# Kernel optimization log

Hardware: AMD Instinct MI355X
Metric: run time of the kernel (lower is better)

The kernel has to match this reference:

```python
import jax, jax.numpy as jnp
import numpy as np

B, T, D, H, KH, HD, F, L, V = 2, 2048, 1024, 16, 4, 64, 4096, 4, 32000
G = H // KH  # num_key_value_groups
EPS = 1e-6
SCALE = HD ** -0.5


def setup_inputs() -> dict:
    key = jax.random.key(0)
    ks = jax.random.split(key, 8)
    std = 0.02
    return {
        "input_ids": jax.random.randint(ks[0], (B, T), 0, V, dtype=jnp.int32),
        "embed_w": jax.random.normal(ks[1], (V, D), jnp.float32) * std,
        "pos_w": jax.random.normal(ks[2], (T, D), jnp.float32) * std,
        "ln1_w": jnp.ones((L, D), jnp.float32),
        "ln2_w": jnp.ones((L, D), jnp.float32),
        "wq": jax.random.normal(ks[3], (L, D, H * HD), jnp.float32) * std,
        "wkv": jax.random.normal(ks[4], (L, D, 2 * KH * HD), jnp.float32) * std,
        "wo": jax.random.normal(ks[5], (L, H * HD, D), jnp.float32) * std,
        "w1": jax.random.normal(ks[6], (L, D, F), jnp.float32) * std,
        "w2": jax.random.normal(ks[7], (L, F, D), jnp.float32) * std,
        "norm_w": jnp.ones((D,), jnp.float32),
    }


def _rmsnorm(x, w):
    return x * jax.lax.rsqrt(jnp.mean(x * x, axis=-1, keepdims=True) + EPS) * w


def reference(input_ids, embed_w, pos_w, ln1_w, ln2_w, wq, wkv, wo, w1, w2, norm_w):
    causal = jnp.tril(jnp.ones((T, T), dtype=bool))  # True = keep
    x = embed_w[input_ids] + pos_w[:T]  # [B,T,D]
    for l in range(L):
        h = _rmsnorm(x, ln1_w[l])
        q = (h @ wq[l]).reshape(B, T, H, HD)
        kv = h @ wkv[l]
        k, v = jnp.split(kv, 2, axis=-1)
        k = jnp.repeat(k.reshape(B, T, KH, HD), G, axis=2)  # GQA repeat_interleave
        v = jnp.repeat(v.reshape(B, T, KH, HD), G, axis=2)
        scores = jnp.einsum("bqhd,bkhd->bhqk", q, k) * SCALE
        scores = jnp.where(causal, scores, -jnp.inf)
        p = jax.nn.softmax(scores, axis=-1)
        o = jnp.einsum("bhqk,bkhd->bqhd", p, v).reshape(B, T, H * HD)
        x = x + o @ wo[l]
        h = _rmsnorm(x, ln2_w[l])
        x = x + jax.nn.gelu(h @ w1[l], approximate=False) @ w2[l]
    x = _rmsnorm(x, norm_w)
    logits = x @ embed_w.T  # tied lm_head
    return logits
```

## Files before the change

kernel.cpp:

```cpp
#include <hip/hip_runtime.h>
#include <hip/hip_bf16.h>

#define DI __device__ __forceinline__

typedef unsigned short u16;
typedef unsigned int u32;
typedef __attribute__((ext_vector_type(8))) short bf16x8;
typedef __attribute__((ext_vector_type(4))) float f32x4;

#define B_   2
#define T_   2048
#define D_   1024
#define H_   16
#define KH_  4
#define HD_  64
#define F_   4096
#define L_   4
#define V_   32000
#define M_   (B_ * T_)
#define QKVN (H_*HD_ + 2*KH_*HD_)

DI u16 f2bf(float f) {
  __hip_bfloat16 h = __float2bfloat16(f);
  return *reinterpret_cast<u16*>(&h);
}

DI float bf2f(u16 b) {
  __hip_bfloat16 h = *reinterpret_cast<__hip_bfloat16*>(&b);
  return __bfloat162float(h);
}

DI void gl_lds16(const void* g, void* l) {
  __builtin_amdgcn_global_load_lds(
      (const __attribute__((address_space(1))) u32*)g,
      (__attribute__((address_space(3))) u32*)l, 16, 0, 0);
}

#define BARRIER() do { asm volatile("" ::: "memory"); __builtin_amdgcn_s_barrier(); asm volatile("" ::: "memory"); } while (0)
#define LGK0()    asm volatile("s_waitcnt lgkmcnt(0)" ::: "memory")
#define VMC(n)    asm volatile("s_waitcnt vmcnt(" #n ")" ::: "memory")
#define PRIO(p)   __builtin_amdgcn_s_setprio(p)

__global__ __launch_bounds__(256) void embed_kernel(const int* __restrict__ ids,
                                                    const float* __restrict__ ew,
                                                    const float* __restrict__ pw,
                                                    float* __restrict__ x) {
  const int row = blockIdx.x;
  const int t = row & (T_ - 1);
  const int id = ids[row];
  float4 e = reinterpret_cast<const float4*>(ew + (size_t)id * D_)[threadIdx.x];
  float4 p = reinterpret_cast<const float4*>(pw + (size_t)t * D_)[threadIdx.x];
  e.x += p.x; e.y += p.y; e.z += p.z; e.w += p.w;
  reinterpret_cast<float4*>(x + (size_t)row * D_)[threadIdx.x] = e;
}

__global__ __launch_bounds__(256) void conv_kernel(const float* __restrict__ W,
                                                   u16* __restrict__ Wb) {
  const size_t i = (size_t)blockIdx.x * 256 + threadIdx.x;
  float4 v = reinterpret_cast<const float4*>(W)[i];
  ushort4 ov;
  ov.x = f2bf(v.x); ov.y = f2bf(v.y); ov.z = f2bf(v.z); ov.w = f2bf(v.w);
  reinterpret_cast<ushort4*>(Wb)[i] = ov;
}

__global__ __launch_bounds__(256) void convt_fused(const float* __restrict__ wq,
                                                   const float* __restrict__ wkv,
                                                   const float* __restrict__ wo,
                                                   const float* __restrict__ w1,
                                                   const float* __restrict__ w2,
                                                   u16* __restrict__ wtq,
                                                   u16* __restrict__ wto,
                                                   u16* __restrict__ wt1,
                                                   u16* __restrict__ wt2) {
  const int t = blockIdx.x;
  const float* W; u16* Wt; int K, N, local;
  if (t < 1024)      { W = wq;  Wt = wtq;               K = 1024; N = 1024; local = t; }
  else if (t < 1536) { W = wkv; Wt = wtq + 1024*1024;   K = 1024; N = 512;  local = t - 1024; }
  else if (t < 2560) { W = wo;  Wt = wto;               K = 1024; N = 1024; local = t - 1536; }
  else if (t < 6656) { W = w1;  Wt = wt1;               K = 1024; N = 4096; local = t - 2560; }
  else               { W = w2;  Wt = wt2;               K = 4096; N = 1024; local = t - 6656; }
  const int nk = K >> 5;
  const int k0 = (local % nk) * 32, n0 = (local / nk) * 32;
  __shared__ float tb[32][33];
  const int tx = threadIdx.x & 31, ty = threadIdx.x >> 5;
  #pragma unroll
  for (int i = 0; i < 4; i++)
    tb[ty + i*8][tx] = W[(size_t)(k0 + ty + i*8) * N + n0 + tx];
  __syncthreads();
  #pragma unroll
  for (int i = 0; i < 4; i++)
    Wt[(size_t)(n0 + ty + i*8) * K + k0 + tx] = f2bf(tb[tx][ty + i*8]);
}

__global__ __launch_bounds__(256) void rmsnorm_kernel(const float* __restrict__ x,
                                                      const float* __restrict__ w,
                                                      u16* __restrict__ out) {
  const int row = blockIdx.x;
  const int tid = threadIdx.x;
  float4 v = reinterpret_cast<const float4*>(x + (size_t)row * D_)[tid];
  float ss = v.x*v.x + v.y*v.y + v.z*v.z + v.w*v.w;
  #pragma unroll
  for (int off = 32; off > 0; off >>= 1) ss += __shfl_down(ss, off, 64);
  __shared__ float red[4];
  if ((tid & 63) == 0) red[tid >> 6] = ss;
  __syncthreads();
  const float tot = red[0] + red[1] + red[2] + red[3];
  const float rstd = rsqrtf(tot * (1.0f / D_) + 1e-6f);
  float4 wv = reinterpret_cast<const float4*>(w)[tid];
  ushort4 ov;
  ov.x = f2bf(v.x * rstd * wv.x);
  ov.y = f2bf(v.y * rstd * wv.y);
  ov.z = f2bf(v.z * rstd * wv.z);
  ov.w = f2bf(v.w * rstd * wv.w);
  reinterpret_cast<ushort4*>(out + (size_t)row * D_)[tid] = ov;
}

template <int EPI>
__global__ __launch_bounds__(256) void gemm_bt(const u16* __restrict__ A,
                                               const u16* __restrict__ Bt,
                                               const float* __restrict__ res,
                                               u16* __restrict__ Cb,
                                               float* __restrict__ Cf,
                                               int M, int N, int K) {
  __shared__ u16 As[128 * 64];
  __shared__ u16 Bs[128 * 64];
  const int tid = threadIdx.x;
  const int n0 = blockIdx.x * 128;
  const int m0 = blockIdx.y * 128;
  const int lane = tid & 63, wave = tid >> 6;
  const int wm = wave >> 1, wn = wave & 1;
  const int l15 = lane & 15, l4 = lane >> 4;
  const int srow = tid >> 3, scol = (tid & 7) * 8;
  const u16* ag = A + (size_t)(m0 + srow) * K + scol;
  const u16* bg = Bt + (size_t)(n0 + srow) * K + scol;
  u16* asd = &As[srow * 64 + scol];
  u16* bsd = &Bs[srow * 64 + scol];
  f32x4 acc[4][4] = {};
  const int nk = K >> 6;
  for (int kt = 0; kt < nk; kt++) {
    const int k0 = kt * 64;
    __syncthreads();
    #pragma unroll
    for (int i = 0; i < 4; i++) gl_lds16(ag + (size_t)i*32*K + k0, asd + i*32*64);
    #pragma unroll
    for (int i = 0; i < 4; i++) gl_lds16(bg + (size_t)i*32*K + k0, bsd + i*32*64);
    __syncthreads();
    #pragma unroll
    for (int s = 0; s < 2; s++) {
      bf16x8 af[4], bfv[4];
      #pragma unroll
      for (int i = 0; i < 4; i++)
        af[i] = *reinterpret_cast<const bf16x8*>(&As[(wm*64 + i*16 + l15)*64 + s*32 + l4*8]);
      #pragma unroll
      for (int j = 0; j < 4; j++)
        bfv[j] = *reinterpret_cast<const bf16x8*>(&Bs[(wn*64 + j*16 + l15)*64 + s*32 + l4*8]);
      #pragma unroll
      for (int i = 0; i < 4; i++)
        #pragma unroll
        for (int j = 0; j < 4; j++)
          acc[i][j] = __builtin_amdgcn_mfma_f32_16x16x32_bf16(bfv[j], af[i], acc[i][j], 0, 0, 0);
    }
  }
  #pragma unroll
  for (int i = 0; i < 4; i++) {
    const int row = m0 + wm*64 + i*16 + l15;
    #pragma unroll
    for (int j = 0; j < 4; j++) {
      const int colb = n0 + wn*64 + j*16 + l4*4;
      const size_t idx = (size_t)row * N + colb;
      const f32x4 v = acc[i][j];
      if (EPI == 0) {
        ushort4 ov;
        ov.x = f2bf(v[0]); ov.y = f2bf(v[1]); ov.z = f2bf(v[2]); ov.w = f2bf(v[3]);
        *reinterpret_cast<ushort4*>(&Cb[idx]) = ov;
      } else {
        const float4 rv = *reinterpret_cast<const float4*>(&res[idx]);
        float4 ov;
        ov.x = v[0] + rv.x; ov.y = v[1] + rv.y; ov.z = v[2] + rv.z; ov.w = v[3] + rv.w;
        *reinterpret_cast<float4*>(&Cf[idx]) = ov;
      }
    }
  }
}

template <int EPI>
__global__ __launch_bounds__(512, 2) void gemm256(const u16* __restrict__ A,
                                                  const u16* __restrict__ Bt,
                                                  u16* __restrict__ Cb,
                                                  float* __restrict__ Cf,
                                                  int M, int N, int K) {
  __shared__ char lds[131072];
  char* const AsB = lds;
  char* const BsB = lds + 65536;
  const int tid = threadIdx.x;
  const int lane = tid & 63, wave = tid >> 6;
  const int wm = wave >> 2, wn = wave & 3;
  const int l15 = lane & 15, l4 = lane >> 4;

  const int nm = M >> 8;
  const int nwg = nm * (N >> 8);
  const int cpx = nwg >> 3;
  const int bid = blockIdx.x;
  const int wg = (bid & 7) * cpx + (bid >> 3);
  const int m0 = (wg % nm) << 8;
  const int n0 = (wg / nm) << 8;

  const u16* const Atile = A + (size_t)m0 * K;
  const u16* const Btile = Bt + (size_t)n0 * K;

  int soff[2][2], pd[2][2];
  #pragma unroll
  for (int h = 0; h < 2; ++h)
    #pragma unroll
    for (int jj = 0; jj < 2; ++jj) {
      const int row = h*128 + jj*64 + (tid >> 3);
      const int sl  = (tid & 7) ^ (row & 7);
      soff[h][jj] = row * K + sl * 8;
      pd[h][jj]   = h*16384 + jj*8192 + tid*16;
    }
  const int swz = (l15 & 7) << 4;
  const int rb0 = l15*128 + ((l4*16)      ^ swz);
  const int rb1 = l15*128 + ((64 + l4*16) ^ swz);

  #define STA(S,H,T) do { const u16* g_ = Atile + (T)*64; char* d_ = AsB + (S)*32768; \
      gl_lds16(g_ + soff[H][0], d_ + pd[H][0]); gl_lds16(g_ + soff[H][1], d_ + pd[H][1]); } while (0)
  #define STB(S,H,T) do { const u16* g_ = Btile + (T)*64; char* d_ = BsB + (S)*32768; \
      gl_lds16(g_ + soff[H][0], d_ + pd[H][0]); gl_lds16(g_ + soff[H][1], d_ + pd[H][1]); } while (0)
  #define RDA(S,GI,RB) (*reinterpret_cast<const bf16x8*>(AsB + (S)*32768 + (GI)*2048 + (RB)))
  #define RDB(S,GJ,RB) (*reinterpret_cast<const bf16x8*>(BsB + (S)*32768 + (GJ)*2048 + (RB)))

  f32x4 acc[8][4] = {};
  bf16x8 Ar[4][2], Br[4][2];

  #define RDA03(S) { _Pragma("unroll") for (int i=0;i<4;++i){ Ar[i][0]=RDA(S,i*2+wm,rb0); Ar[i][1]=RDA(S,i*2+wm,rb1);} }
  #define RDA47(S) { _Pragma("unroll") for (int i=0;i<4;++i){ Ar[i][0]=RDA(S,(i+4)*2+wm,rb0); Ar[i][1]=RDA(S,(i+4)*2+wm,rb1);} }
  #define RDB01(S) { _Pragma("unroll") for (int j=0;j<2;++j){ Br[j][0]=RDB(S,j*4+wn,rb0); Br[j][1]=RDB(S,j*4+wn,rb1);} }
  #define RDB23(S) { _Pragma("unroll") for (int j=2;j<4;++j){ Br[j][0]=RDB(S,j*4+wn,rb0); Br[j][1]=RDB(S,j*4+wn,rb1);} }
  #define MFQ(IO,JL) { _Pragma("unroll") for (int i=0;i<4;++i) _Pragma("unroll") for (int jj=0;jj<2;++jj) { \
      acc[(IO)+i][(JL)+jj] = __builtin_amdgcn_mfma_f32_16x16x32_bf16(Br[(JL)+jj][0], Ar[i][0], acc[(IO)+i][(JL)+jj],0,0,0); \
      acc[(IO)+i][(JL)+jj] = __builtin_amdgcn_mfma_f32_16x16x32_bf16(Br[(JL)+jj][1], Ar[i][1], acc[(IO)+i][(JL)+jj],0,0,0); } }

  STA(0,0,0); STA(0,1,0); STB(0,0,0); STB(0,1,0);
  VMC(4);
  STA(1,0,1); STB(1,0,1); STB(1,1,1);
  VMC(6);
  BARRIER();

  const int niter = K >> 7;
  for (int it = 0; it < niter; ++it) {
    const int t0 = it*2, t1 = t0 + 1;
    const bool pf = (it + 1 < niter);
    RDA03(0); RDB01(0); STA(1,1,t1);
    BARRIER(); LGK0(); PRIO(1); MFQ(0,0); PRIO(0); BARRIER();
    RDB23(0); if (pf) STA(0,0,t0+2);
    BARRIER(); LGK0(); PRIO(1); MFQ(0,2); PRIO(0); BARRIER();
    RDA47(0); if (pf) STB(0,0,t0+2);
    BARRIER(); LGK0(); PRIO(1); MFQ(4,0); PRIO(0); BARRIER();
    if (pf) { STB(0,1,t0+2); VMC(6); } else { VMC(0); }
    BARRIER(); PRIO(1); MFQ(4,2); PRIO(0); BARRIER();
    RDA03(1); RDB01(1); if (pf) STA(0,1,t0+2);
    BARRIER(); LGK0(); PRIO(1); MFQ(0,0); PRIO(0); BARRIER();
    RDB23(1); if (pf) STA(1,0,t1+2);
    BARRIER(); LGK0(); PRIO(1); MFQ(0,2); PRIO(0); BARRIER();
    RDA47(1); if (pf) STB(1,0,t1+2);
    BARRIER(); LGK0(); PRIO(1); MFQ(4,0); PRIO(0); BARRIER();
    if (pf) { STB(1,1,t1+2); VMC(6); }
    BARRIER(); PRIO(1); MFQ(4,2); PRIO(0); BARRIER();
  }

  #pragma unroll
  for (int i = 0; i < 8; ++i) {
    const int row = m0 + (i*2 + wm)*16 + l15;
    #pragma unroll
    for (int j = 0; j < 4; ++j) {
      const int colb = n0 + (j*4 + wn)*16 + l4*4;
      const f32x4 v = acc[i][j];
      if (EPI == 0) {
        *reinterpret_cast<f32x4*>(&Cf[(size_t)row * N + colb]) = v;
      } else {
        ushort4 ov;
        #pragma unroll
        for (int rr = 0; rr < 4; ++rr) {
          const float g = 0.5f * v[rr] * (1.0f + erff(v[rr] * 0.70710678118f));
          ((u16*)&ov)[rr] = f2bf(g);
        }
        *reinterpret_cast<ushort4*>(&Cb[(size_t)row * N + colb]) = ov;
      }
    }
  }
  #undef STA
  #undef STB
  #undef RDA
  #undef RDB
  #undef RDA03
  #undef RDA47
  #undef RDB01
  #undef RDB23
  #undef MFQ
}

__global__ __launch_bounds__(256) void attn_kernel(const u16* __restrict__ qkv,
                                                   u16* __restrict__ o) {
  const int qt = blockIdx.x;
  const int h  = blockIdx.y;
  const int b  = blockIdx.z;
  const int kh = h / (H_ / KH_);
  __shared__ u16 Ks[2][64 * 64];
  __shared__ u16 Vt[64 * 66];
  __shared__ u16 Pl[4][16 * 68];
  const int tid = threadIdx.x, lane = tid & 63, wave = tid >> 6;
  const int l15 = lane & 15, l4 = lane >> 4;
  const size_t Mrow = (size_t)b * T_;

  bf16x8 qf[2];
  {
    const u16* qp = qkv + (Mrow + qt*64 + wave*16 + l15) * QKVN + h*HD_ + l4*8;
    qf[0] = *reinterpret_cast<const bf16x8*>(qp);
    qf[1] = *reinterpret_cast<const bf16x8*>(qp + 32);
    #pragma unroll
    for (int s = 0; s < 2; s++)
      #pragma unroll
      for (int j = 0; j < 8; j++)
        qf[s][j] = (short)f2bf(bf2f((u16)qf[s][j]) * 0.125f);
  }
  float m_run[4], l_run[4];
  f32x4 oacc[4] = {};
  #pragma unroll
  for (int r = 0; r < 4; r++) { m_run[r] = -1e30f; l_run[r] = 0.0f; }

  const int srow = tid >> 3, scol = (tid & 7) * 8;
  const int vp = (tid >> 3) * 2;
  const int vd = (tid & 7) * 8;
  const u16* const kbase = qkv + Mrow * QKVN + D_ + kh*HD_;
  const u16* const vbase = kbase + KH_*HD_;

  {
    const u16* kg = kbase + (size_t)srow * QKVN + scol;
    gl_lds16(kg, &Ks[0][srow*64 + scol]);
    gl_lds16(kg + 32*QKVN, &Ks[0][(srow+32)*64 + scol]);
    const u16* vg = vbase + (size_t)vp * QKVN + vd;
    bf16x8 v0 = *reinterpret_cast<const bf16x8*>(vg);
    bf16x8 v1 = *reinterpret_cast<const bf16x8*>(vg + QKVN);
    #pragma unroll
    for (int j = 0; j < 8; j++) {
      const u32 pk = (u32)(u16)v0[j] | ((u32)(u16)v1[j] << 16);
      *reinterpret_cast<u32*>(&Vt[(vd + j)*66 + vp]) = pk;
    }
  }
  __syncthreads();

  for (int kt = 0; kt <= qt; kt++) {
    const int cur = kt & 1;
    const bool pf = kt < qt;
    bf16x8 v0n, v1n;
    if (pf) {
      const u16* kg = kbase + (size_t)((kt+1)*64 + srow) * QKVN + scol;
      gl_lds16(kg, &Ks[1-cur][srow*64 + scol]);
      gl_lds16(kg + 32*QKVN, &Ks[1-cur][(srow+32)*64 + scol]);
      const u16* vg = vbase + (size_t)((kt+1)*64 + vp) * QKVN + vd;
      v0n = *reinterpret_cast<const bf16x8*>(vg);
      v1n = *reinterpret_cast<const bf16x8*>(vg + QKVN);
    }

    f32x4 sa[4] = {};
    #pragma unroll
    for (int s = 0; s < 2; s++)
      #pragma unroll
      for (int n = 0; n < 4; n++) {
        bf16x8 kf = *reinterpret_cast<const bf16x8*>(&Ks[cur][(n*16 + l15)*64 + s*32 + l4*8]);
        sa[n] = __builtin_amdgcn_mfma_f32_16x16x32_bf16(qf[s], kf, sa[n], 0, 0, 0);
      }
    if (kt == qt) {
      const int qloc = wave*16 + l4*4;
      #pragma unroll
      for (int n = 0; n < 4; n++) {
        const int kloc = n*16 + l15;
        #pragma unroll
        for (int r = 0; r < 4; r++)
          if (kloc > qloc + r) sa[n][r] = -1e30f;
      }
    }
    float mx[4];
    #pragma unroll
    for (int r = 0; r < 4; r++)
      mx[r] = fmaxf(fmaxf(sa[0][r], sa[1][r]), fmaxf(sa[2][r], sa[3][r]));
    #pragma unroll
    for (int off = 1; off < 16; off <<= 1)
      #pragma unroll
      for (int r = 0; r < 4; r++)
        mx[r] = fmaxf(mx[r], __shfl_xor(mx[r], off, 64));
    float alpha[4], rs[4];
    #pragma unroll
    for (int r = 0; r < 4; r++) {
      const float nm = fmaxf(m_run[r], mx[r]);
      alpha[r] = __expf(m_run[r] - nm);
      m_run[r] = nm;
      rs[r] = 0.0f;
    }
    u16* pw = &Pl[wave][0];
    #pragma unroll
    for (int n = 0; n < 4; n++)
      #pragma unroll
      for (int r = 0; r < 4; r++) {
        const float p = __expf(sa[n][r] - m_run[r]);
        rs[r] += p;
        pw[(l4*4 + r)*68 + n*16 + l15] = f2bf(p);
      }
    #pragma unroll
    for (int off = 1; off < 16; off <<= 1)
      #pragma unroll
      for (int r = 0; r < 4; r++)
        rs[r] += __shfl_xor(rs[r], off, 64);
    #pragma unroll
    for (int r = 0; r < 4; r++) l_run[r] = l_run[r]*alpha[r] + rs[r];
    #pragma unroll
    for (int n = 0; n < 4; n++)
      #pragma unroll
      for (int r = 0; r < 4; r++) oacc[n][r] *= alpha[r];

    asm volatile("s_waitcnt lgkmcnt(0)" ::: "memory");
    #pragma unroll
    for (int s = 0; s < 2; s++) {
      bf16x8 pa = *reinterpret_cast<const bf16x8*>(&Pl[wave][l15*68 + s*32 + l4*8]);
      #pragma unroll
      for (int n = 0; n < 4; n++) {
        bf16x8 vb = *reinterpret_cast<const bf16x8*>(&Vt[(n*16 + l15)*66 + s*32 + l4*8]);
        oacc[n] = __builtin_amdgcn_mfma_f32_16x16x32_bf16(pa, vb, oacc[n], 0, 0, 0);
      }
    }
    __syncthreads();
    if (pf) {
      #pragma unroll
      for (int j = 0; j < 8; j++) {
        const u32 pk = (u32)(u16)v0n[j] | ((u32)(u16)v1n[j] << 16);
        *reinterpret_cast<u32*>(&Vt[(vd + j)*66 + vp]) = pk;
      }
      __syncthreads();
    }
  }
  #pragma unroll
  for (int n = 0; n < 4; n++)
    #pragma unroll
    for (int r = 0; r < 4; r++) {
      const float ov = oacc[n][r] / l_run[r];
      const size_t row = Mrow + qt*64 + wave*16 + l4*4 + r;
      o[row * (size_t)(H_*HD_) + h*HD_ + n*16 + l15] = f2bf(ov);
    }
}

#define OFF_X     0ull
#define OFF_H     16777216ull
#define OFF_QKV   25165824ull
#define OFF_O     37748736ull
#define OFF_U     46137344ull
#define OFF_WTQ   79691776ull
#define OFF_WTO   82837504ull
#define OFF_WT1   84934656ull
#define OFF_WT2   93323264ull
#define OFF_EBF   101711872ull

extern "C" void kernel_launch(void* const* d_in, const int* in_sizes, int n_in,
                              void* d_out, int out_size, void* d_ws, size_t ws_size,
                              hipStream_t stream) {
  const int*   ids = (const int*)  d_in[0];
  const float* ew  = (const float*)d_in[1];
  const float* pw  = (const float*)d_in[2];
  const float* ln1 = (const float*)d_in[3];
  const float* ln2 = (const float*)d_in[4];
  const float* wq  = (const float*)d_in[5];
  const float* wkv = (const float*)d_in[6];
  const float* wo  = (const float*)d_in[7];
  const float* w1  = (const float*)d_in[8];
  const float* w2  = (const float*)d_in[9];
  const float* nw  = (const float*)d_in[10];
  float* out = (float*)d_out;

  char* ws = (char*)d_ws;
  float* x   = (float*)(ws + OFF_X);
  u16*   h   = (u16*)  (ws + OFF_H);
  u16*   qkv = (u16*)  (ws + OFF_QKV);
  u16*   o   = (u16*)  (ws + OFF_O);
  u16*   u   = (u16*)  (ws + OFF_U);
  u16*   wtq = (u16*)  (ws + OFF_WTQ);
  u16*   wto = (u16*)  (ws + OFF_WTO);
  u16*   wt1 = (u16*)  (ws + OFF_WT1);
  u16*   wt2 = (u16*)  (ws + OFF_WT2);
  u16*   ebf = (u16*)  (ws + OFF_EBF);

  embed_kernel<<<M_, 256, 0, stream>>>(ids, ew, pw, x);
  conv_kernel<<<(V_*D_/4)/256, 256, 0, stream>>>(ew, ebf);

  for (int l = 0; l < L_; l++) {
    convt_fused<<<10752, 256, 0, stream>>>(
        wq  + (size_t)l*D_*(H_*HD_),
        wkv + (size_t)l*D_*(2*KH_*HD_),
        wo  + (size_t)l*(H_*HD_)*D_,
        w1  + (size_t)l*D_*F_,
        w2  + (size_t)l*F_*D_,
        wtq, wto, wt1, wt2);

    rmsnorm_kernel<<<M_, 256, 0, stream>>>(x, ln1 + (size_t)l*D_, h);
    gemm_bt<0><<<dim3(QKVN/128, M_/128), 256, 0, stream>>>(h, wtq, nullptr, qkv, nullptr, M_, QKVN, D_);
    attn_kernel<<<dim3(T_/64, H_, B_), 256, 0, stream>>>(qkv, o);
    gemm_bt<1><<<dim3(D_/128, M_/128), 256, 0, stream>>>(o, wto, x, nullptr, x, M_, D_, H_*HD_);
    rmsnorm_kernel<<<M_, 256, 0, stream>>>(x, ln2 + (size_t)l*D_, h);
    gemm256<1><<<dim3((F_/256)*(M_/256)), 512, 0, stream>>>(h, wt1, u, nullptr, M_, F_, D_);
    gemm_bt<1><<<dim3(D_/128, M_/128), 256, 0, stream>>>(u, wt2, x, nullptr, x, M_, D_, F_);
  }

  rmsnorm_kernel<<<M_, 256, 0, stream>>>(x, nw, h);
  gemm256<0><<<dim3((V_/256)*(M_/256)), 512, 0, stream>>>(h, ebf, nullptr, out, M_, V_, D_);
}
```

Measured before the change: 1.807 ms.

## Double attention query tile to 128 rows, use exp2 softmax with lazy rescaling

The attention kernel now runs 512 threads per block covering 128 query rows (8 waves), so each staged 64-key K/V tile is shared by twice as many query rows. The causal loop and mask are rewritten for the larger tile, and the K/V staging is spread over the extra threads. Softmax now folds log2(e) into the Q scale and uses exp2f. Rescaling of the accumulator is skipped unless a wave's running max grows by more than 8, which cuts per-tile multiplies but lets unnormalised p values reach up to 2^8 before bf16 rounding. The block count halves and the diagonal tiles do more fully masked work, which lowers occupancy and parallelism.

```diff
diff --git a/kernel.cpp b/kernel.cpp
--- a/kernel.cpp
+++ b/kernel.cpp
@@ -6,6 +6,7 @@
 typedef unsigned short u16;
 typedef unsigned int u32;
 typedef __attribute__((ext_vector_type(8))) short bf16x8;
+typedef __attribute__((ext_vector_type(4))) short bf16x4;
 typedef __attribute__((ext_vector_type(4))) float f32x4;
 
 #define B_   2
@@ -299,7 +300,7 @@
   #undef MFQ
 }
 
-__global__ __launch_bounds__(256) void attn_kernel(const u16* __restrict__ qkv,
+__global__ __launch_bounds__(512) void attn_kernel(const u16* __restrict__ qkv,
                                                    u16* __restrict__ o) {
   const int qt = blockIdx.x;
   const int h  = blockIdx.y;
@@ -307,21 +308,21 @@
   const int kh = h / (H_ / KH_);
   __shared__ u16 Ks[2][64 * 64];
   __shared__ u16 Vt[64 * 66];
-  __shared__ u16 Pl[4][16 * 68];
+  __shared__ u16 Pl[8][16 * 68];
   const int tid = threadIdx.x, lane = tid & 63, wave = tid >> 6;
   const int l15 = lane & 15, l4 = lane >> 4;
   const size_t Mrow = (size_t)b * T_;
 
   bf16x8 qf[2];
   {
-    const u16* qp = qkv + (Mrow + qt*64 + wave*16 + l15) * QKVN + h*HD_ + l4*8;
+    const u16* qp = qkv + (Mrow + qt*128 + wave*16 + l15) * QKVN + h*HD_ + l4*8;
     qf[0] = *reinterpret_cast<const bf16x8*>(qp);
     qf[1] = *reinterpret_cast<const bf16x8*>(qp + 32);
     #pragma unroll
     for (int s = 0; s < 2; s++)
       #pragma unroll
       for (int j = 0; j < 8; j++)
-        qf[s][j] = (short)f2bf(bf2f((u16)qf[s][j]) * 0.125f);
+        qf[s][j] = (short)f2bf(bf2f((u16)qf[s][j]) * 0.18033688f);
   }
   float m_run[4], l_run[4];
   f32x4 oacc[4] = {};
@@ -329,37 +330,35 @@
   for (int r = 0; r < 4; r++) { m_run[r] = -1e30f; l_run[r] = 0.0f; }
 
   const int srow = tid >> 3, scol = (tid & 7) * 8;
-  const int vp = (tid >> 3) * 2;
-  const int vd = (tid & 7) * 8;
+  const int vp = (tid >> 4) * 2;
+  const int vd = (tid & 15) * 4;
   const u16* const kbase = qkv + Mrow * QKVN + D_ + kh*HD_;
   const u16* const vbase = kbase + KH_*HD_;
 
   {
-    const u16* kg = kbase + (size_t)srow * QKVN + scol;
-    gl_lds16(kg, &Ks[0][srow*64 + scol]);
-    gl_lds16(kg + 32*QKVN, &Ks[0][(srow+32)*64 + scol]);
+    gl_lds16(kbase + (size_t)srow * QKVN + scol, &Ks[0][srow*64 + scol]);
     const u16* vg = vbase + (size_t)vp * QKVN + vd;
-    bf16x8 v0 = *reinterpret_cast<const bf16x8*>(vg);
-    bf16x8 v1 = *reinterpret_cast<const bf16x8*>(vg + QKVN);
-    #pragma unroll
-    for (int j = 0; j < 8; j++) {
+    bf16x4 v0 = *reinterpret_cast<const bf16x4*>(vg);
+    bf16x4 v1 = *reinterpret_cast<const bf16x4*>(vg + QKVN);
+    #pragma unroll
+    for (int j = 0; j < 4; j++) {
       const u32 pk = (u32)(u16)v0[j] | ((u32)(u16)v1[j] << 16);
       *reinterpret_cast<u32*>(&Vt[(vd + j)*66 + vp]) = pk;
     }
   }
   __syncthreads();
 
-  for (int kt = 0; kt <= qt; kt++) {
+  const int nkt = 2*qt + 2;
+  for (int kt = 0; kt < nkt; kt++) {
     const int cur = kt & 1;
-    const bool pf = kt < qt;
-    bf16x8 v0n, v1n;
+    const bool pf = kt + 1 < nkt;
+    bf16x4 v0n, v1n;
     if (pf) {
-      const u16* kg = kbase + (size_t)((kt+1)*64 + srow) * QKVN + scol;
-      gl_lds16(kg, &Ks[1-cur][srow*64 + scol]);
-      gl_lds16(kg + 32*QKVN, &Ks[1-cur][(srow+32)*64 + scol]);
+      gl_lds16(kbase + (size_t)((kt+1)*64 + srow) * QKVN + scol,
+               &Ks[1-cur][srow*64 + scol]);
       const u16* vg = vbase + (size_t)((kt+1)*64 + vp) * QKVN + vd;
-      v0n = *reinterpret_cast<const bf16x8*>(vg);
-      v1n = *reinterpret_cast<const bf16x8*>(vg + QKVN);
+      v0n = *reinterpret_cast<const bf16x4*>(vg);
+      v1n = *reinterpret_cast<const bf16x4*>(vg + QKVN);
     }
 
     f32x4 sa[4] = {};
@@ -370,11 +369,11 @@
         bf16x8 kf = *reinterpret_cast<const bf16x8*>(&Ks[cur][(n*16 + l15)*64 + s*32 + l4*8]);
         sa[n] = __builtin_amdgcn_mfma_f32_16x16x32_bf16(qf[s], kf, sa[n], 0, 0, 0);
       }
-    if (kt == qt) {
+    if (kt >= 2*qt) {
       const int qloc = wave*16 + l4*4;
       #pragma unroll
       for (int n = 0; n < 4; n++) {
-        const int kloc = n*16 + l15;
+        const int kloc = kt*64 - qt*128 + n*16 + l15;
         #pragma unroll
         for (int r = 0; r < 4; r++)
           if (kloc > qloc + r) sa[n][r] = -1e30f;
@@ -389,20 +388,27 @@
       #pragma unroll
       for (int r = 0; r < 4; r++)
         mx[r] = fmaxf(mx[r], __shfl_xor(mx[r], off, 64));
-    float alpha[4], rs[4];
-    #pragma unroll
-    for (int r = 0; r < 4; r++) {
-      const float nm = fmaxf(m_run[r], mx[r]);
-      alpha[r] = __expf(m_run[r] - nm);
-      m_run[r] = nm;
-      rs[r] = 0.0f;
-    }
+    bool need = false;
+    #pragma unroll
+    for (int r = 0; r < 4; r++) need = need || (mx[r] - m_run[r] > 8.0f);
+    if (__any((int)need)) {
+      #pragma unroll
+      for (int r = 0; r < 4; r++) {
+        const float nm = fmaxf(m_run[r], mx[r]);
+        const float alpha = exp2f(m_run[r] - nm);
+        m_run[r] = nm;
+        l_run[r] *= alpha;
+        #pragma unroll
+        for (int n = 0; n < 4; n++) oacc[n][r] *= alpha;
+      }
+    }
+    float rs[4] = {0.f, 0.f, 0.f, 0.f};
     u16* pw = &Pl[wave][0];
     #pragma unroll
     for (int n = 0; n < 4; n++)
       #pragma unroll
       for (int r = 0; r < 4; r++) {
-        const float p = __expf(sa[n][r] - m_run[r]);
+        const float p = exp2f(sa[n][r] - m_run[r]);
         rs[r] += p;
         pw[(l4*4 + r)*68 + n*16 + l15] = f2bf(p);
       }
@@ -412,11 +418,7 @@
       for (int r = 0; r < 4; r++)
         rs[r] += __shfl_xor(rs[r], off, 64);
     #pragma unroll
-    for (int r = 0; r < 4; r++) l_run[r] = l_run[r]*alpha[r] + rs[r];
-    #pragma unroll
-    for (int n = 0; n < 4; n++)
-      #pragma unroll
-      for (int r = 0; r < 4; r++) oacc[n][r] *= alpha[r];
+    for (int r = 0; r < 4; r++) l_run[r] += rs[r];
 
     asm volatile("s_waitcnt lgkmcnt(0)" ::: "memory");
     #pragma unroll
@@ -431,7 +433,7 @@
     __syncthreads();
     if (pf) {
       #pragma unroll
-      for (int j = 0; j < 8; j++) {
+      for (int j = 0; j < 4; j++) {
         const u32 pk = (u32)(u16)v0n[j] | ((u32)(u16)v1n[j] << 16);
         *reinterpret_cast<u32*>(&Vt[(vd + j)*66 + vp]) = pk;
       }
@@ -443,7 +445,7 @@
     #pragma unroll
     for (int r = 0; r < 4; r++) {
       const float ov = oacc[n][r] / l_run[r];
-      const size_t row = Mrow + qt*64 + wave*16 + l4*4 + r;
+      const size_t row = Mrow + qt*128 + wave*16 + l4*4 + r;
       o[row * (size_t)(H_*HD_) + h*HD_ + n*16 + l15] = f2bf(ov);
     }
 }
@@ -501,7 +503,7 @@
 
     rmsnorm_kernel<<<M_, 256, 0, stream>>>(x, ln1 + (size_t)l*D_, h);
     gemm_bt<0><<<dim3(QKVN/128, M_/128), 256, 0, stream>>>(h, wtq, nullptr, qkv, nullptr, M_, QKVN, D_);
-    attn_kernel<<<dim3(T_/64, H_, B_), 256, 0, stream>>>(qkv, o);
+    attn_kernel<<<dim3(T_/128, H_, B_), 512, 0, stream>>>(qkv, o);
     gemm_bt<1><<<dim3(D_/128, M_/128), 256, 0, stream>>>(o, wto, x, nullptr, x, M_, D_, H_*HD_);
     rmsnorm_kernel<<<M_, 256, 0, stream>>>(x, ln2 + (size_t)l*D_, h);
     gemm256<1><<<dim3((F_/256)*(M_/256)), 512, 0, stream>>>(h, wt1, u, nullptr, M_, F_, D_);
```

Result: no change. 1.778 ms (-1.6%).
